# Kernel optimization log

Measured on AMD Instinct MI355X. Metric: run time of the kernel, lower is better.

The kernel has to match this reference:

```python
import jax, jax.numpy as jnp
import numpy as np

NL, NH, H, FF, V, P = 12, 12, 768, 3072, 30522, 512
B, L, S = 4, 512, 8
DH = H // NH


def _layer_norm(x, g, b, eps=1e-12):
    m = x.mean(-1, keepdims=True)
    v = jnp.mean((x - m) ** 2, axis=-1, keepdims=True)
    return (x - m) * jax.lax.rsqrt(v + eps) * g + b


def setup_inputs() -> dict:
    key = jax.random.key(0)
    ks = iter(jax.random.split(key, 40))
    pm = lambda shape: jax.random.normal(next(ks), shape, jnp.float32) * 0.02
    inp = {
        'word_emb': pm((V, H)), 'pos_emb': pm((P, H)), 'type_emb': pm((2, H)),
        'emb_ln_g': jnp.ones((H,), jnp.float32), 'emb_ln_b': jnp.zeros((H,), jnp.float32),
        'Wq': pm((NL, H, H)), 'bq': jnp.zeros((NL, H), jnp.float32),
        'Wk': pm((NL, H, H)), 'bk': jnp.zeros((NL, H), jnp.float32),
        'Wv': pm((NL, H, H)), 'bv': jnp.zeros((NL, H), jnp.float32),
        'Wo': pm((NL, H, H)), 'bo': jnp.zeros((NL, H), jnp.float32),
        'attn_ln_g': jnp.ones((NL, H), jnp.float32), 'attn_ln_b': jnp.zeros((NL, H), jnp.float32),
        'W1': pm((NL, H, FF)), 'b1': jnp.zeros((NL, FF), jnp.float32),
        'W2': pm((NL, FF, H)), 'b2': jnp.zeros((NL, H), jnp.float32),
        'ffn_ln_g': jnp.ones((NL, H), jnp.float32), 'ffn_ln_b': jnp.zeros((NL, H), jnp.float32),
        'fc_w': pm((H,)), 'fc_b': jnp.zeros((), jnp.float32),
    }
    inp['input_ids'] = jax.random.randint(next(ks), (B, L), 0, V)
    inp['token_type_ids'] = jnp.zeros((B, L), jnp.int32)
    # valid-length prefix attention_mask and sorted bos_locations (history = 64)
    vl = np.array([384 + 16 * (i % 8) for i in range(B)])
    hist = 64
    am = (np.arange(L)[None, :] < vl[:, None]).astype(np.int32)
    bos = np.stack([hist + (np.arange(S) * (v - hist)) // S for v in vl]).astype(np.int64)
    inp['attention_mask'] = jnp.asarray(am)
    inp['bos_locations'] = jnp.asarray(bos)
    return inp


def _forward(word_emb, pos_emb, type_emb, emb_ln_g, emb_ln_b,
             Wq, bq, Wk, bk, Wv, bv, Wo, bo, attn_ln_g, attn_ln_b,
             W1, b1, W2, b2, ffn_ln_g, ffn_ln_b, fc_w, fc_b,
             input_ids, token_type_ids, attention_mask, bos_locations):
    Bs, Ls = input_ids.shape
    t = jnp.arange(Ls)
    valid_len = attention_mask.sum(-1)                       # [B]
    hist = bos_locations[:, 0]                               # [B] history length
    # segment id per token: number of bos positions <= t, minus 1 (-1 in history)
    seg = (bos_locations[:, :, None] <= t[None, None, :]).sum(1) - 1   # [B,L]
    valid = t[None, :] < valid_len[:, None]                  # [B,L]
    # block-diagonal candidate attention mask (history rows/cols fully visible)
    p = t[None, :, None]
    q = t[None, None, :]
    hist_pq = (p < hist[:, None, None]) | (q < hist[:, None, None])
    same_seg = seg[:, :, None] == seg[:, None, :]
    mask = valid[:, :, None] & valid[:, None, :] & (hist_pq | same_seg)  # [B,L,L]
    bias = jnp.where(mask, 0.0, -10000.0).astype(jnp.float32)[:, None, :, :]  # [B,1,L,L]

    # BERT embeddings
    x = word_emb[input_ids] + pos_emb[t][None] + type_emb[token_type_ids]
    x = _layer_norm(x, emb_ln_g, emb_ln_b)
    scale = 1.0 / jnp.sqrt(jnp.asarray(DH, x.dtype))

    for l in range(NL):
        qh = (x @ Wq[l] + bq[l]).reshape(Bs, Ls, NH, DH)
        kh = (x @ Wk[l] + bk[l]).reshape(Bs, Ls, NH, DH)
        vh = (x @ Wv[l] + bv[l]).reshape(Bs, Ls, NH, DH)
        scores = jnp.einsum('bqhd,bkhd->bhqk', qh, kh) * scale + bias
        probs = jax.nn.softmax(scores, axis=-1)
        ctx = jnp.einsum('bhqk,bkhd->bqhd', probs, vh).reshape(Bs, Ls, H)
        x = _layer_norm(x + ctx @ Wo[l] + bo[l], attn_ln_g[l], attn_ln_b[l])
        h = jax.nn.gelu(x @ W1[l] + b1[l], approximate=False)
        x = _layer_norm(x + h @ W2[l] + b2[l], ffn_ln_g[l], ffn_ln_b[l])

    # variable-length segment mean pooling via membership matmul
    starts = bos_locations                                   # [B,S]
    ends = jnp.concatenate([bos_locations[:, 1:], valid_len[:, None]], axis=1)
    memb = ((t[None, None, :] >= starts[:, :, None]) &
            (t[None, None, :] < ends[:, :, None])).astype(x.dtype)        # [B,S,L]
    pooled = jnp.einsum('bsl,bld->bsd', memb, x) / memb.sum(-1, keepdims=True)
    logits = pooled @ fc_w + fc_b                            # [B,S]
    return jnp.squeeze(logits)


def reference(word_emb, pos_emb, type_emb, emb_ln_g, emb_ln_b,
              Wq, bq, Wk, bk, Wv, bv, Wo, bo, attn_ln_g, attn_ln_b,
              W1, b1, W2, b2, ffn_ln_g, ffn_ln_b, fc_w, fc_b,
              input_ids, token_type_ids, attention_mask, bos_locations):
    return _forward(word_emb, pos_emb, type_emb, emb_ln_g, emb_ln_b,
                    Wq, bq, Wk, bk, Wv, bv, Wo, bo, attn_ln_g, attn_ln_b,
                    W1, b1, W2, b2, ffn_ln_g, ffn_ln_b, fc_w, fc_b,
                    input_ids, token_type_ids, attention_mask, bos_locations)
```

## Files before the change

kernel.cpp:

```cpp
#include <hip/hip_runtime.h>
#include <math.h>

#define HH 768
#define FF 3072
#define NL 12
#define NH 12
#define DH 64
#define BB 4
#define LL 512
#define SS 8
#define MM (BB*LL)
#define WQSZ (HH*HH)
#define W1SZ (HH*FF)
#define LWB 7077888
#define OFF_WO 1769472
#define OFF_W1 2359296
#define OFF_W2 4718592

typedef short bf16x8 __attribute__((ext_vector_type(8)));
typedef float f32x4 __attribute__((ext_vector_type(4)));

__device__ inline ushort f2b(float f) {
  unsigned u = __float_as_uint(f);
  unsigned r = (u + 0x7FFFu + ((u >> 16) & 1u)) >> 16;
  return (ushort)r;
}
__device__ inline float b2f(ushort b) {
  return __uint_as_float(((unsigned)b) << 16);
}

__device__ inline void swz_xy(int& x, int& y) {
  int gx = gridDim.x, gy = gridDim.y;
  int flat = blockIdx.x + blockIdx.y * gx;
  int nwg = gx * gy;
  int q = nwg >> 3, r = nwg & 7;
  int xcd = flat & 7, off = flat >> 3;
  int wgid = (xcd < r ? xcd * (q + 1) : r * (q + 1) + (xcd - r) * q) + off;
  x = wgid / gy; y = wgid - x * gy;
}

__global__ void prep_kernel(const int* __restrict__ am, const int* __restrict__ bos,
                            int* __restrict__ seg, int* __restrict__ vl) {
  int b = blockIdx.x;
  int t = threadIdx.x;
  __shared__ int red[512];
  red[t] = am[b*LL + t];
  __syncthreads();
  for (int off = 256; off > 0; off >>= 1) {
    if (t < off) red[t] += red[t+off];
    __syncthreads();
  }
  if (t == 0) vl[b] = red[0];
  int cnt = 0;
  #pragma unroll
  for (int s = 0; s < SS; s++) cnt += (bos[b*SS + s] <= t) ? 1 : 0;
  seg[b*LL + t] = cnt - 1;
}

__global__ __launch_bounds__(256) void embed_ln_kernel(
    const float* __restrict__ word_emb, const float* __restrict__ pos_emb,
    const float* __restrict__ type_emb, const float* __restrict__ g,
    const float* __restrict__ bta, const int* __restrict__ ids,
    const int* __restrict__ tts, float* __restrict__ x, ushort* __restrict__ xb)
{
  int row = blockIdx.x;
  int l = row & (LL-1);
  int t = threadIdx.x;
  int id = ids[row];
  int ty = tts[row];
  float4 v = {0.f,0.f,0.f,0.f};
  float s = 0.f, sq = 0.f;
  int c = t << 2;
  if (t < 192) {
    float4 a = *(const float4*)&word_emb[(size_t)id*HH + c];
    float4 p = *(const float4*)&pos_emb[l*HH + c];
    float4 ttv = *(const float4*)&type_emb[ty*HH + c];
    v.x = a.x+p.x+ttv.x; v.y = a.y+p.y+ttv.y; v.z = a.z+p.z+ttv.z; v.w = a.w+p.w+ttv.w;
    s = v.x+v.y+v.z+v.w;
    sq = v.x*v.x+v.y*v.y+v.z*v.z+v.w*v.w;
  }
  __shared__ float rs[256], rq[256];
  rs[t] = s; rq[t] = sq;
  __syncthreads();
  for (int off = 128; off > 0; off >>= 1) {
    if (t < off) { rs[t] += rs[t+off]; rq[t] += rq[t+off]; }
    __syncthreads();
  }
  float mean = rs[0] / HH;
  float var  = rq[0] / HH - mean*mean;
  float inv  = rsqrtf(var + 1e-12f);
  if (t < 192) {
    float4 gv = *(const float4*)&g[c];
    float4 bv = *(const float4*)&bta[c];
    float4 o;
    o.x = (v.x-mean)*inv*gv.x + bv.x;
    o.y = (v.y-mean)*inv*gv.y + bv.y;
    o.z = (v.z-mean)*inv*gv.z + bv.z;
    o.w = (v.w-mean)*inv*gv.w + bv.w;
    *(float4*)&x[(size_t)row*HH + c] = o;
    ushort4 ob = { f2b(o.x), f2b(o.y), f2b(o.z), f2b(o.w) };
    *(ushort4*)&xb[(size_t)row*HH + c] = ob;
  }
}

template<int NP>
__global__ __launch_bounds__(256) void add_ln_kernel(
    const float* __restrict__ xin, const ushort* __restrict__ y,
    const float* __restrict__ g, const float* __restrict__ bta,
    float* __restrict__ xout, ushort* __restrict__ xb)
{
  int row = blockIdx.x;
  int t = threadIdx.x;
  float4 v = {0.f,0.f,0.f,0.f};
  float s = 0.f, sq = 0.f;
  int c = t << 2;
  size_t ix = (size_t)row*HH + c;
  if (t < 192) {
    v = *(const float4*)&xin[ix];
    #pragma unroll
    for (int p = 0; p < NP; p++) {
      ushort4 yb = *(const ushort4*)&y[(size_t)p*MM*HH + ix];
      v.x += b2f(yb.x); v.y += b2f(yb.y); v.z += b2f(yb.z); v.w += b2f(yb.w);
    }
    s = v.x+v.y+v.z+v.w;
    sq = v.x*v.x+v.y*v.y+v.z*v.z+v.w*v.w;
  }
  __shared__ float rs[256], rq[256];
  rs[t] = s; rq[t] = sq;
  __syncthreads();
  for (int off = 128; off > 0; off >>= 1) {
    if (t < off) { rs[t] += rs[t+off]; rq[t] += rq[t+off]; }
    __syncthreads();
  }
  float mean = rs[0] / HH;
  float var  = rq[0] / HH - mean*mean;
  float inv  = rsqrtf(var + 1e-12f);
  if (t < 192) {
    float4 gv = *(const float4*)&g[c];
    float4 bv = *(const float4*)&bta[c];
    float4 o;
    o.x = (v.x-mean)*inv*gv.x + bv.x;
    o.y = (v.y-mean)*inv*gv.y + bv.y;
    o.z = (v.z-mean)*inv*gv.z + bv.z;
    o.w = (v.w-mean)*inv*gv.w + bv.w;
    *(float4*)&xout[ix] = o;
    ushort4 ob = { f2b(o.x), f2b(o.y), f2b(o.z), f2b(o.w) };
    *(ushort4*)&xb[ix] = ob;
  }
}

__global__ __launch_bounds__(256) void convw_all_kernel(
    const float* __restrict__ Wq, const float* __restrict__ Wk,
    const float* __restrict__ Wv, const float* __restrict__ Wo,
    const float* __restrict__ W1, const float* __restrict__ W2,
    ushort* __restrict__ wbuf)
{
  int idx = blockIdx.x;
  int l = idx / 1728;
  int t0 = idx % 1728;
  size_t base = (size_t)l * LWB;
  const float* src; ushort* dst; int Nsrc, dstK, k0, n0src, n0dst;
  if (t0 < 432) {
    int nt = t0 / 12, kt = t0 % 12;
    int z = nt / 12, ntl = nt % 12;
    src = (z == 0 ? Wq : z == 1 ? Wk : Wv) + (size_t)l*WQSZ;
    dst = wbuf + base;
    Nsrc = HH; dstK = HH; k0 = kt*64; n0src = ntl*64; n0dst = nt*64;
  } else if (t0 < 576) {
    int t = t0 - 432; int nt = t / 12, kt = t % 12;
    src = Wo + (size_t)l*WQSZ;
    dst = wbuf + base + OFF_WO;
    Nsrc = HH; dstK = HH; k0 = kt*64; n0src = n0dst = nt*64;
  } else if (t0 < 1152) {
    int t = t0 - 576; int nt = t / 12, kt = t % 12;
    src = W1 + (size_t)l*W1SZ;
    dst = wbuf + base + OFF_W1;
    Nsrc = FF; dstK = HH; k0 = kt*64; n0src = n0dst = nt*64;
  } else {
    int t = t0 - 1152; int nt = t / 48, kt = t % 48;
    src = W2 + (size_t)l*W1SZ;
    dst = wbuf + base + OFF_W2;
    Nsrc = HH; dstK = FF; k0 = kt*64; n0src = n0dst = nt*64;
  }
  __shared__ ushort tt[64][66];
  int tid = threadIdx.x;
  int kr = tid >> 4;
  int nn0 = (tid & 15) << 2;
  #pragma unroll
  for (int i = 0; i < 4; i++) {
    int k = kr + i*16;
    float4 v = *(const float4*)&src[(size_t)(k0+k)*Nsrc + n0src + nn0];
    ushort2 lo = { f2b(v.x), f2b(v.y) };
    ushort2 hi = { f2b(v.z), f2b(v.w) };
    *(ushort2*)&tt[k][nn0]     = lo;
    *(ushort2*)&tt[k][nn0 + 2] = hi;
  }
  __syncthreads();
  ushort* dtile = dst + ((size_t)(n0dst >> 6)*(dstK >> 6) + (k0 >> 6)) * 4096;
  #pragma unroll
  for (int it = 0; it < 2; it++) {
    int n  = it*32 + (tid >> 3);
    int kc = (tid & 7) << 3;
    ushort tmp8[8];
    #pragma unroll
    for (int j = 0; j < 8; j++) tmp8[j] = tt[kc + j][n];
    *(uint4*)&dtile[n*64 + kc] = *(const uint4*)tmp8;
  }
}

template<int MODE>
__global__ __launch_bounds__(256) void gemm_bt(
    const ushort* __restrict__ A, const ushort* __restrict__ Bt,
    const float* __restrict__ ba, const float* __restrict__ bb,
    const float* __restrict__ bc, float* __restrict__ Cf,
    ushort* __restrict__ Cb, int M, int N, int K)
{
  __shared__ __align__(16) ushort As[2][128*64];
  __shared__ __align__(16) ushort Bs[2][64*64];
  const int tid = threadIdx.x;
  const int lane = tid & 63, wid = tid >> 6;
  const int wm = wid >> 1, wn = wid & 1;
  int bx, by; swz_xy(bx, by);
  const int m0 = by * 128, n0 = bx * 64;
  int kbeg = 0, kcnt = K;
  if (MODE == 2) { kcnt = K >> 1; kbeg = blockIdx.z * kcnt; }
  const int NT = kcnt >> 6;
  const ushort* Bpanel = Bt + (size_t)(n0 >> 6) * (K >> 6) * 4096;

  auto STAGE = [&](int buf, int k0) {
    #pragma unroll
    for (int j = 0; j < 4; j++) {
      int c = j*256 + tid;
      int r = c >> 3;
      int kk = ((c & 7) ^ (r & 7)) << 3;
      __builtin_amdgcn_global_load_lds(
        (const __attribute__((address_space(1))) void*)(A + (size_t)(m0+r)*K + k0 + kk),
        (__attribute__((address_space(3))) void*)(&As[buf][c*8]), 16, 0, 0);
    }
    const ushort* btile = Bpanel + (size_t)(k0 >> 6) * 4096;
    #pragma unroll
    for (int j = 0; j < 2; j++) {
      int c = j*256 + tid;
      int r = c >> 3;
      int kk = ((c & 7) ^ (r & 7)) << 3;
      __builtin_amdgcn_global_load_lds(
        (const __attribute__((address_space(1))) void*)(btile + r*64 + kk),
        (__attribute__((address_space(3))) void*)(&Bs[buf][c*8]), 16, 0, 0);
    }
  };

  f32x4 acc[4][2] = {};
  STAGE(0, kbeg);
  __syncthreads();
  int cur = 0;
  for (int t = 0; t < NT; ++t) {
    if (t + 1 < NT) STAGE(cur ^ 1, kbeg + (t+1)*64);
    bf16x8 af[4][2], bfv[2][2];
    #pragma unroll
    for (int mi = 0; mi < 4; mi++) {
      int row = wm*64 + mi*16 + (lane & 15);
      #pragma unroll
      for (int ks = 0; ks < 2; ks++) {
        int kb = (ks*64 + ((lane >> 4) << 4)) ^ ((row & 7) << 4);
        af[mi][ks] = *(const bf16x8*)((const char*)&As[cur][0] + row*128 + kb);
      }
    }
    #pragma unroll
    for (int ni = 0; ni < 2; ni++) {
      int row = wn*32 + ni*16 + (lane & 15);
      #pragma unroll
      for (int ks = 0; ks < 2; ks++) {
        int kb = (ks*64 + ((lane >> 4) << 4)) ^ ((row & 7) << 4);
        bfv[ni][ks] = *(const bf16x8*)((const char*)&Bs[cur][0] + row*128 + kb);
      }
    }
    #pragma unroll
    for (int ks = 0; ks < 2; ks++)
      #pragma unroll
      for (int mi = 0; mi < 4; mi++)
        #pragma unroll
        for (int ni = 0; ni < 2; ni++)
          acc[mi][ni] = __builtin_amdgcn_mfma_f32_16x16x32_bf16(af[mi][ks], bfv[ni][ks], acc[mi][ni], 0, 0, 0);
    __syncthreads();
    cur ^= 1;
  }

  #pragma unroll
  for (int mi = 0; mi < 4; mi++) {
    #pragma unroll
    for (int ni = 0; ni < 2; ni++) {
      int col = n0 + wn*32 + ni*16 + (lane & 15);
      if (MODE == 0) {
        int z = n0 / 768;
        int cc = col - z*768;
        float bvv = (z == 0 ? ba : z == 1 ? bb : bc)[cc];
        #pragma unroll
        for (int r = 0; r < 4; r++) {
          int row = m0 + wm*64 + mi*16 + (lane >> 4)*4 + r;
          Cb[(size_t)z*MM*HH + (size_t)row*HH + cc] = f2b(acc[mi][ni][r] + bvv);
        }
      } else if (MODE == 1) {
        float bvv = ba[col];
        #pragma unroll
        for (int r = 0; r < 4; r++) {
          int row = m0 + wm*64 + mi*16 + (lane >> 4)*4 + r;
          float v = acc[mi][ni][r] + bvv;
          v = 0.5f * v * (1.0f + erff(v * 0.70710678118654752f));
          Cb[(size_t)row*N + col] = f2b(v);
        }
      } else {
        float bvv = (blockIdx.z == 0) ? ba[col] : 0.f;
        #pragma unroll
        for (int r = 0; r < 4; r++) {
          int row = m0 + wm*64 + mi*16 + (lane >> 4)*4 + r;
          Cb[(size_t)blockIdx.z*M*N + (size_t)row*N + col] = f2b(acc[mi][ni][r] + bvv);
        }
      }
    }
  }
}

__global__ __launch_bounds__(256) void attn_mfma_kernel(
    const ushort* __restrict__ Q, const ushort* __restrict__ Kp, const ushort* __restrict__ Vp,
    ushort* __restrict__ ctx, const int* __restrict__ seg, const int* __restrict__ vl,
    const int* __restrict__ bos)
{
  const int q0 = blockIdx.x * 64;
  const int h  = blockIdx.y;
  const int b  = blockIdx.z;
  const int tid = threadIdx.x;
  const int lane = tid & 63;
  const int wid = tid >> 6;

  __shared__ __align__(16) char Ks[2][8192];
  __shared__ __align__(16) char Vt[2][8192];
  __shared__ __align__(16) char Ps[4][2048];
  __shared__ int segk[2][64];

  const int qrow_frag = q0 + wid*16 + (lane & 15);
  bf16x8 qf[2];
  #pragma unroll
  for (int c = 0; c < 2; c++)
    qf[c] = *(const bf16x8*)&Q[((size_t)(b*LL + qrow_frag))*HH + h*DH + 32*c + (lane >> 4)*8];

  const int vlb  = vl[b];
  const int hist = bos[b*SS];
  int segq[4]; bool qvalid[4], qhist[4];
  #pragma unroll
  for (int r = 0; r < 4; r++) {
    int qg = q0 + wid*16 + (lane >> 4)*4 + r;
    segq[r]   = seg[b*LL + qg];
    qvalid[r] = qg < vlb;
    qhist[r]  = qg < hist;
  }

  float mrow[4], lrow[4];
  #pragma unroll
  for (int r = 0; r < 4; r++) { mrow[r] = -1e30f; lrow[r] = 0.f; }
  f32x4 Oacc[4] = {};

  uint4 kreg0, kreg1, vreg0, vreg1;
  int sreg = 0;

  auto LOADT = [&](int k0) {
    int rk = tid >> 3;
    int c8 = (tid & 7) * 8;
    kreg0 = *(const uint4*)&Kp[((size_t)(b*LL + k0 + rk))*HH + h*DH + c8];
    kreg1 = *(const uint4*)&Kp[((size_t)(b*LL + k0 + rk + 32))*HH + h*DH + c8];
    vreg0 = *(const uint4*)&Vp[((size_t)(b*LL + k0 + lane))*HH + h*DH + wid*8];
    vreg1 = *(const uint4*)&Vp[((size_t)(b*LL + k0 + lane))*HH + h*DH + wid*8 + 32];
    if (tid < 64) sreg = seg[b*LL + k0 + tid];
  };
  auto STORET = [&](int buf) {
    int rk = tid >> 3;
    int c8 = (tid & 7) * 8;
    *(uint4*)(Ks[buf] + (rk*128 + ((c8*2) ^ ((rk & 7) << 4)))) = kreg0;
    int rk2 = rk + 32;
    *(uint4*)(Ks[buf] + (rk2*128 + ((c8*2) ^ ((rk2 & 7) << 4)))) = kreg1;
    const ushort* pv0 = (const ushort*)&vreg0;
    const ushort* pv1 = (const ushort*)&vreg1;
    #pragma unroll
    for (int j = 0; j < 8; j++) {
      int d  = wid*8 + j;
      *(ushort*)(Vt[buf] + (d*128 + ((lane*2) ^ ((d & 7) << 4)))) = pv0[j];
      int d2 = d + 32;
      *(ushort*)(Vt[buf] + (d2*128 + ((lane*2) ^ ((d2 & 7) << 4)))) = pv1[j];
    }
    if (tid < 64) segk[buf][tid] = sreg;
  };

  LOADT(0);
  STORET(0);
  __syncthreads();

  for (int kt = 0; kt < 8; kt++) {
    const int cur = kt & 1;
    const int k0 = kt * 64;
    if (kt < 7) LOADT(k0 + 64);
    __builtin_amdgcn_sched_barrier(0);

    f32x4 sacc[4] = {};
    #pragma unroll
    for (int t = 0; t < 4; t++) {
      int krow = (lane & 15) + 16*t;
      #pragma unroll
      for (int c = 0; c < 2; c++) {
        bf16x8 kf = *(const bf16x8*)(Ks[cur] + (krow*128 +
                      (((32*c + (lane >> 4)*8)*2) ^ ((krow & 7) << 4))));
        sacc[t] = __builtin_amdgcn_mfma_f32_16x16x32_bf16(qf[c], kf, sacc[t], 0, 0, 0);
      }
    }

    #pragma unroll
    for (int t = 0; t < 4; t++) {
      int kg = k0 + (lane & 15) + 16*t;
      bool kvalid = kg < vlb;
      bool khist  = kg < hist;
      int  sk     = segk[cur][(lane & 15) + 16*t];
      #pragma unroll
      for (int r = 0; r < 4; r++) {
        bool ok = qvalid[r] && kvalid && (khist || qhist[r] || (segq[r] == sk));
        sacc[t][r] = sacc[t][r]*0.125f + (ok ? 0.f : -10000.f);
      }
    }

    float scl[4];
    #pragma unroll
    for (int r = 0; r < 4; r++) {
      float rm = fmaxf(fmaxf(sacc[0][r], sacc[1][r]), fmaxf(sacc[2][r], sacc[3][r]));
      rm = fmaxf(rm, __shfl_xor(rm, 1));
      rm = fmaxf(rm, __shfl_xor(rm, 2));
      rm = fmaxf(rm, __shfl_xor(rm, 4));
      rm = fmaxf(rm, __shfl_xor(rm, 8));
      float mnew = (rm > mrow[r] + 8.f) ? rm : mrow[r];
      scl[r] = (mnew == mrow[r]) ? 1.f : __expf(mrow[r] - mnew);
      float rsum = 0.f;
      #pragma unroll
      for (int t = 0; t < 4; t++) {
        float p = __expf(sacc[t][r] - mnew);
        sacc[t][r] = p;
        rsum += p;
      }
      rsum += __shfl_xor(rsum, 1);
      rsum += __shfl_xor(rsum, 2);
      rsum += __shfl_xor(rsum, 4);
      rsum += __shfl_xor(rsum, 8);
      mrow[r] = mnew;
      lrow[r] = lrow[r]*scl[r] + rsum;
    }

    char* Pl = Ps[wid];
    #pragma unroll
    for (int t = 0; t < 4; t++) {
      #pragma unroll
      for (int r = 0; r < 4; r++) {
        int q = (lane >> 4)*4 + r;
        int k = (lane & 15) + 16*t;
        *(ushort*)(Pl + (q*128 + ((k*2) ^ ((q & 7) << 4)))) = f2b(sacc[t][r]);
      }
    }
    asm volatile("s_waitcnt lgkmcnt(0)" ::: "memory");
    bf16x8 pf[2];
    #pragma unroll
    for (int c = 0; c < 2; c++) {
      int q = lane & 15;
      int k = 32*c + (lane >> 4)*8;
      pf[c] = *(const bf16x8*)(Pl + (q*128 + ((k*2) ^ ((q & 7) << 4))));
    }

    bool needscale = (scl[0] != 1.f) | (scl[1] != 1.f) | (scl[2] != 1.f) | (scl[3] != 1.f);
    #pragma unroll
    for (int nt = 0; nt < 4; nt++) {
      if (needscale) {
        #pragma unroll
        for (int r = 0; r < 4; r++) Oacc[nt][r] *= scl[r];
      }
      int d = (lane & 15) + 16*nt;
      #pragma unroll
      for (int c = 0; c < 2; c++) {
        int k = 32*c + (lane >> 4)*8;
        bf16x8 vf = *(const bf16x8*)(Vt[cur] + (d*128 + ((k*2) ^ ((d & 7) << 4))));
        Oacc[nt] = __builtin_amdgcn_mfma_f32_16x16x32_bf16(pf[c], vf, Oacc[nt], 0, 0, 0);
      }
    }

    if (kt < 7) STORET(cur ^ 1);
    __syncthreads();
  }

  #pragma unroll
  for (int nt = 0; nt < 4; nt++) {
    #pragma unroll
    for (int r = 0; r < 4; r++) {
      int q = q0 + wid*16 + (lane >> 4)*4 + r;
      int d = h*DH + (lane & 15) + 16*nt;
      ctx[(size_t)(b*LL + q)*HH + d] = f2b(Oacc[nt][r] / lrow[r]);
    }
  }
}

__global__ __launch_bounds__(256) void rowdot_kernel(const float* __restrict__ x,
                                                     const float* __restrict__ w,
                                                     float* __restrict__ rd) {
  int row = blockIdx.x;
  int t = threadIdx.x;
  float s = 0.f;
  if (t < 192) {
    int c = t << 2;
    float4 xv = *(const float4*)&x[(size_t)row*HH + c];
    float4 wv = *(const float4*)&w[c];
    s = xv.x*wv.x + xv.y*wv.y + xv.z*wv.z + xv.w*wv.w;
  }
  __shared__ float red[256];
  red[t] = s;
  __syncthreads();
  for (int off = 128; off > 0; off >>= 1) {
    if (t < off) red[t] += red[t+off];
    __syncthreads();
  }
  if (t == 0) rd[row] = red[0];
}

__global__ void logits_kernel(const float* __restrict__ rd, const int* __restrict__ bos,
                              const int* __restrict__ vl, const float* __restrict__ fcb,
                              float* __restrict__ out) {
  int i = threadIdx.x;
  if (i >= BB*SS) return;
  int b = i / SS, s = i % SS;
  int start = bos[b*SS + s];
  int end   = (s == SS-1) ? vl[b] : bos[b*SS + s + 1];
  float sum = 0.f;
  for (int t = start; t < end; t++) sum += rd[b*LL + t];
  out[i] = sum / (float)(end - start) + fcb[0];
}

extern "C" void kernel_launch(void* const* d_in, const int* in_sizes, int n_in,
                              void* d_out, int out_size, void* d_ws, size_t ws_size,
                              hipStream_t stream) {
  const float* word_emb  = (const float*)d_in[0];
  const float* pos_emb   = (const float*)d_in[1];
  const float* type_emb  = (const float*)d_in[2];
  const float* emb_ln_g  = (const float*)d_in[3];
  const float* emb_ln_b  = (const float*)d_in[4];
  const float* Wq        = (const float*)d_in[5];
  const float* bq        = (const float*)d_in[6];
  const float* Wk        = (const float*)d_in[7];
  const float* bk        = (const float*)d_in[8];
  const float* Wv        = (const float*)d_in[9];
  const float* bv        = (const float*)d_in[10];
  const float* Wo        = (const float*)d_in[11];
  const float* bo        = (const float*)d_in[12];
  const float* attn_ln_g = (const float*)d_in[13];
  const float* attn_ln_b = (const float*)d_in[14];
  const float* W1        = (const float*)d_in[15];
  const float* b1        = (const float*)d_in[16];
  const float* W2        = (const float*)d_in[17];
  const float* b2        = (const float*)d_in[18];
  const float* ffn_ln_g  = (const float*)d_in[19];
  const float* ffn_ln_b  = (const float*)d_in[20];
  const float* fc_w      = (const float*)d_in[21];
  const float* fc_b      = (const float*)d_in[22];
  const int* input_ids   = (const int*)d_in[23];
  const int* token_type  = (const int*)d_in[24];
  const int* am          = (const int*)d_in[25];
  const int* bos         = (const int*)d_in[26];
  float* out = (float*)d_out;

  char* w = (char*)d_ws;
  float*  x       = (float*)w;  w += (size_t)MM*HH*4;
  ushort* tmpb    = (ushort*)w; w += (size_t)2*MM*HH*2;
  ushort* qkv_bf  = (ushort*)w; w += (size_t)3*MM*HH*2;
  ushort* x_bf    = (ushort*)w; w += (size_t)MM*HH*2;
  ushort* ctx_bf  = (ushort*)w; w += (size_t)MM*HH*2;
  ushort* hbuf_bf = (ushort*)w; w += (size_t)MM*FF*2;
  ushort* wbuf    = (ushort*)w; w += (size_t)NL*LWB*2;
  float*  rd      = (float*)w;  w += (size_t)MM*4;
  int*    seg     = (int*)w;    w += (size_t)MM*4;
  int*    vl      = (int*)w;    w += 64;

  prep_kernel<<<BB, 512, 0, stream>>>(am, bos, seg, vl);
  convw_all_kernel<<<NL*1728, 256, 0, stream>>>(Wq, Wk, Wv, Wo, W1, W2, wbuf);
  embed_ln_kernel<<<MM, 256, 0, stream>>>(word_emb, pos_emb, type_emb,
                                          emb_ln_g, emb_ln_b, input_ids, token_type, x, x_bf);

  dim3 gqkv(2304/64, MM/128);
  dim3 g_ff1(FF/64, MM/128);
  dim3 g_sk(HH/64, MM/128, 2);
  dim3 gattn(LL/64, NH, BB);

  for (int l = 0; l < NL; l++) {
    const ushort* Wqkv_t = wbuf + (size_t)l*LWB;
    const ushort* Wo_t   = wbuf + (size_t)l*LWB + OFF_WO;
    const ushort* W1_t   = wbuf + (size_t)l*LWB + OFF_W1;
    const ushort* W2_t   = wbuf + (size_t)l*LWB + OFF_W2;

    gemm_bt<0><<<gqkv, 256, 0, stream>>>(x_bf, Wqkv_t,
        bq + (size_t)l*HH, bk + (size_t)l*HH, bv + (size_t)l*HH,
        nullptr, qkv_bf, MM, 2304, HH);

    attn_mfma_kernel<<<gattn, 256, 0, stream>>>(qkv_bf, qkv_bf + (size_t)MM*HH,
                                                qkv_bf + (size_t)2*MM*HH, ctx_bf, seg, vl, bos);

    gemm_bt<2><<<g_sk, 256, 0, stream>>>(ctx_bf, Wo_t,
        bo + (size_t)l*HH, nullptr, nullptr, nullptr, tmpb, MM, HH, HH);

    add_ln_kernel<2><<<MM, 256, 0, stream>>>(x, tmpb, attn_ln_g + (size_t)l*HH,
                                             attn_ln_b + (size_t)l*HH, x, x_bf);

    gemm_bt<1><<<g_ff1, 256, 0, stream>>>(x_bf, W1_t,
        b1 + (size_t)l*FF, nullptr, nullptr, nullptr, hbuf_bf, MM, FF, HH);

    gemm_bt<2><<<g_sk, 256, 0, stream>>>(hbuf_bf, W2_t,
        b2 + (size_t)l*HH, nullptr, nullptr, nullptr, tmpb, MM, HH, FF);

    add_ln_kernel<2><<<MM, 256, 0, stream>>>(x, tmpb, ffn_ln_g + (size_t)l*HH,
                                             ffn_ln_b + (size_t)l*HH, x, x_bf);
  }

  rowdot_kernel<<<MM, 256, 0, stream>>>(x, fc_w, rd);
  logits_kernel<<<1, 64, 0, stream>>>(rd, bos, vl, fc_b, out);
}
```

Measured before the change: 1.439 ms.

## Split-K into four fp32 partials for Wo/W2 GEMMs and per-layer weight conversion

```diff
diff --git a/kernel.cpp b/kernel.cpp
--- a/kernel.cpp
+++ b/kernel.cpp
@@ -24,9 +24,6 @@
   unsigned u = __float_as_uint(f);
   unsigned r = (u + 0x7FFFu + ((u >> 16) & 1u)) >> 16;
   return (ushort)r;
-}
-__device__ inline float b2f(ushort b) {
-  return __uint_as_float(((unsigned)b) << 16);
 }
 
 __device__ inline void swz_xy(int& x, int& y) {
@@ -105,7 +102,7 @@
 
 template<int NP>
 __global__ __launch_bounds__(256) void add_ln_kernel(
-    const float* __restrict__ xin, const ushort* __restrict__ y,
+    const float* __restrict__ xin, const float* __restrict__ y,
     const float* __restrict__ g, const float* __restrict__ bta,
     float* __restrict__ xout, ushort* __restrict__ xb)
 {
@@ -119,8 +116,8 @@
     v = *(const float4*)&xin[ix];
     #pragma unroll
     for (int p = 0; p < NP; p++) {
-      ushort4 yb = *(const ushort4*)&y[(size_t)p*MM*HH + ix];
-      v.x += b2f(yb.x); v.y += b2f(yb.y); v.z += b2f(yb.z); v.w += b2f(yb.w);
+      float4 yv = *(const float4*)&y[(size_t)p*MM*HH + ix];
+      v.x += yv.x; v.y += yv.y; v.z += yv.z; v.w += yv.w;
     }
     s = v.x+v.y+v.z+v.w;
     sq = v.x*v.x+v.y*v.y+v.z*v.z+v.w*v.w;
@@ -149,37 +146,31 @@
   }
 }
 
-__global__ __launch_bounds__(256) void convw_all_kernel(
+__global__ __launch_bounds__(256) void convw_layer_kernel(
     const float* __restrict__ Wq, const float* __restrict__ Wk,
     const float* __restrict__ Wv, const float* __restrict__ Wo,
     const float* __restrict__ W1, const float* __restrict__ W2,
-    ushort* __restrict__ wbuf)
+    ushort* __restrict__ wl)
 {
-  int idx = blockIdx.x;
-  int l = idx / 1728;
-  int t0 = idx % 1728;
-  size_t base = (size_t)l * LWB;
+  int t0 = blockIdx.x;
   const float* src; ushort* dst; int Nsrc, dstK, k0, n0src, n0dst;
   if (t0 < 432) {
     int nt = t0 / 12, kt = t0 % 12;
     int z = nt / 12, ntl = nt % 12;
-    src = (z == 0 ? Wq : z == 1 ? Wk : Wv) + (size_t)l*WQSZ;
-    dst = wbuf + base;
+    src = (z == 0 ? Wq : z == 1 ? Wk : Wv);
+    dst = wl;
     Nsrc = HH; dstK = HH; k0 = kt*64; n0src = ntl*64; n0dst = nt*64;
   } else if (t0 < 576) {
     int t = t0 - 432; int nt = t / 12, kt = t % 12;
-    src = Wo + (size_t)l*WQSZ;
-    dst = wbuf + base + OFF_WO;
+    src = Wo; dst = wl + OFF_WO;
     Nsrc = HH; dstK = HH; k0 = kt*64; n0src = n0dst = nt*64;
   } else if (t0 < 1152) {
     int t = t0 - 576; int nt = t / 12, kt = t % 12;
-    src = W1 + (size_t)l*W1SZ;
-    dst = wbuf + base + OFF_W1;
+    src = W1; dst = wl + OFF_W1;
     Nsrc = FF; dstK = HH; k0 = kt*64; n0src = n0dst = nt*64;
   } else {
     int t = t0 - 1152; int nt = t / 48, kt = t % 48;
-    src = W2 + (size_t)l*W1SZ;
-    dst = wbuf + base + OFF_W2;
+    src = W2; dst = wl + OFF_W2;
     Nsrc = HH; dstK = FF; k0 = kt*64; n0src = n0dst = nt*64;
   }
   __shared__ ushort tt[64][66];
@@ -223,7 +214,7 @@
   int bx, by; swz_xy(bx, by);
   const int m0 = by * 128, n0 = bx * 64;
   int kbeg = 0, kcnt = K;
-  if (MODE == 2) { kcnt = K >> 1; kbeg = blockIdx.z * kcnt; }
+  if (MODE == 2) { kcnt = K >> 2; kbeg = blockIdx.z * kcnt; }
   const int NT = kcnt >> 6;
   const ushort* Bpanel = Bt + (size_t)(n0 >> 6) * (K >> 6) * 4096;
 
@@ -313,7 +304,7 @@
         #pragma unroll
         for (int r = 0; r < 4; r++) {
           int row = m0 + wm*64 + mi*16 + (lane >> 4)*4 + r;
-          Cb[(size_t)blockIdx.z*M*N + (size_t)row*N + col] = f2b(acc[mi][ni][r] + bvv);
+          Cf[(size_t)blockIdx.z*M*N + (size_t)row*N + col] = acc[mi][ni][r] + bvv;
         }
       }
     }
@@ -568,7 +559,7 @@
 
   char* w = (char*)d_ws;
   float*  x       = (float*)w;  w += (size_t)MM*HH*4;
-  ushort* tmpb    = (ushort*)w; w += (size_t)2*MM*HH*2;
+  float*  tmp     = (float*)w;  w += (size_t)4*MM*HH*4;
   ushort* qkv_bf  = (ushort*)w; w += (size_t)3*MM*HH*2;
   ushort* x_bf    = (ushort*)w; w += (size_t)MM*HH*2;
   ushort* ctx_bf  = (ushort*)w; w += (size_t)MM*HH*2;
@@ -579,13 +570,17 @@
   int*    vl      = (int*)w;    w += 64;
 
   prep_kernel<<<BB, 512, 0, stream>>>(am, bos, seg, vl);
-  convw_all_kernel<<<NL*1728, 256, 0, stream>>>(Wq, Wk, Wv, Wo, W1, W2, wbuf);
+  for (int l = 0; l < NL; l++)
+    convw_layer_kernel<<<1728, 256, 0, stream>>>(
+        Wq + (size_t)l*WQSZ, Wk + (size_t)l*WQSZ, Wv + (size_t)l*WQSZ,
+        Wo + (size_t)l*WQSZ, W1 + (size_t)l*W1SZ, W2 + (size_t)l*W1SZ,
+        wbuf + (size_t)l*LWB);
   embed_ln_kernel<<<MM, 256, 0, stream>>>(word_emb, pos_emb, type_emb,
                                           emb_ln_g, emb_ln_b, input_ids, token_type, x, x_bf);
 
   dim3 gqkv(2304/64, MM/128);
   dim3 g_ff1(FF/64, MM/128);
-  dim3 g_sk(HH/64, MM/128, 2);
+  dim3 g_sk(HH/64, MM/128, 4);
   dim3 gattn(LL/64, NH, BB);
 
   for (int l = 0; l < NL; l++) {
@@ -602,18 +597,18 @@
                                                 qkv_bf + (size_t)2*MM*HH, ctx_bf, seg, vl, bos);
 
     gemm_bt<2><<<g_sk, 256, 0, stream>>>(ctx_bf, Wo_t,
-        bo + (size_t)l*HH, nullptr, nullptr, nullptr, tmpb, MM, HH, HH);
-
-    add_ln_kernel<2><<<MM, 256, 0, stream>>>(x, tmpb, attn_ln_g + (size_t)l*HH,
+        bo + (size_t)l*HH, nullptr, nullptr, tmp, nullptr, MM, HH, HH);
+
+    add_ln_kernel<4><<<MM, 256, 0, stream>>>(x, tmp, attn_ln_g + (size_t)l*HH,
                                              attn_ln_b + (size_t)l*HH, x, x_bf);
 
     gemm_bt<1><<<g_ff1, 256, 0, stream>>>(x_bf, W1_t,
         b1 + (size_t)l*FF, nullptr, nullptr, nullptr, hbuf_bf, MM, FF, HH);
 
     gemm_bt<2><<<g_sk, 256, 0, stream>>>(hbuf_bf, W2_t,
-        b2 + (size_t)l*HH, nullptr, nullptr, nullptr, tmpb, MM, HH, FF);
-
-    add_ln_kernel<2><<<MM, 256, 0, stream>>>(x, tmpb, ffn_ln_g + (size_t)l*HH,
+        b2 + (size_t)l*HH, nullptr, nullptr, tmp, nullptr, MM, HH, FF);
+
+    add_ln_kernel<4><<<MM, 256, 0, stream>>>(x, tmp, ffn_ln_g + (size_t)l*HH,
                                              ffn_ln_b + (size_t)l*HH, x, x_bf);
   }
 
```

New measurement: 1.442 ms. Within noise of the previous version (+0.2%).

## Deepen GEMM prefetch pipeline, use 4-way split-K with fp32 partials

Applied to the files above, without the earlier changes.

```diff
diff --git a/kernel.cpp b/kernel.cpp
--- a/kernel.cpp
+++ b/kernel.cpp
@@ -24,9 +24,6 @@
   unsigned u = __float_as_uint(f);
   unsigned r = (u + 0x7FFFu + ((u >> 16) & 1u)) >> 16;
   return (ushort)r;
-}
-__device__ inline float b2f(ushort b) {
-  return __uint_as_float(((unsigned)b) << 16);
 }
 
 __device__ inline void swz_xy(int& x, int& y) {
@@ -105,7 +102,7 @@
 
 template<int NP>
 __global__ __launch_bounds__(256) void add_ln_kernel(
-    const float* __restrict__ xin, const ushort* __restrict__ y,
+    const float* __restrict__ xin, const float* __restrict__ y,
     const float* __restrict__ g, const float* __restrict__ bta,
     float* __restrict__ xout, ushort* __restrict__ xb)
 {
@@ -119,8 +116,8 @@
     v = *(const float4*)&xin[ix];
     #pragma unroll
     for (int p = 0; p < NP; p++) {
-      ushort4 yb = *(const ushort4*)&y[(size_t)p*MM*HH + ix];
-      v.x += b2f(yb.x); v.y += b2f(yb.y); v.z += b2f(yb.z); v.w += b2f(yb.w);
+      float4 yv = *(const float4*)&y[(size_t)p*MM*HH + ix];
+      v.x += yv.x; v.y += yv.y; v.z += yv.z; v.w += yv.w;
     }
     s = v.x+v.y+v.z+v.w;
     sq = v.x*v.x+v.y*v.y+v.z*v.z+v.w*v.w;
@@ -223,7 +220,7 @@
   int bx, by; swz_xy(bx, by);
   const int m0 = by * 128, n0 = bx * 64;
   int kbeg = 0, kcnt = K;
-  if (MODE == 2) { kcnt = K >> 1; kbeg = blockIdx.z * kcnt; }
+  if (MODE == 2) { kcnt = K >> 2; kbeg = blockIdx.z * kcnt; }
   const int NT = kcnt >> 6;
   const ushort* Bpanel = Bt + (size_t)(n0 >> 6) * (K >> 6) * 4096;
 
@@ -251,10 +248,15 @@
 
   f32x4 acc[4][2] = {};
   STAGE(0, kbeg);
-  __syncthreads();
-  int cur = 0;
+  if (NT > 1) STAGE(1, kbeg + 64);
   for (int t = 0; t < NT; ++t) {
-    if (t + 1 < NT) STAGE(cur ^ 1, kbeg + (t+1)*64);
+    const int cur = t & 1;
+    if (t + 1 < NT) asm volatile("s_waitcnt vmcnt(6)" ::: "memory");
+    else            asm volatile("s_waitcnt vmcnt(0)" ::: "memory");
+    __builtin_amdgcn_sched_barrier(0);
+    __builtin_amdgcn_s_barrier();
+    __builtin_amdgcn_sched_barrier(0);
+
     bf16x8 af[4][2], bfv[2][2];
     #pragma unroll
     for (int mi = 0; mi < 4; mi++) {
@@ -281,8 +283,12 @@
         #pragma unroll
         for (int ni = 0; ni < 2; ni++)
           acc[mi][ni] = __builtin_amdgcn_mfma_f32_16x16x32_bf16(af[mi][ks], bfv[ni][ks], acc[mi][ni], 0, 0, 0);
-    __syncthreads();
-    cur ^= 1;
+
+    asm volatile("s_waitcnt lgkmcnt(0)" ::: "memory");
+    __builtin_amdgcn_sched_barrier(0);
+    __builtin_amdgcn_s_barrier();
+    __builtin_amdgcn_sched_barrier(0);
+    if (t + 2 < NT) STAGE(cur, kbeg + (t + 2) * 64);
   }
 
   #pragma unroll
@@ -313,7 +319,7 @@
         #pragma unroll
         for (int r = 0; r < 4; r++) {
           int row = m0 + wm*64 + mi*16 + (lane >> 4)*4 + r;
-          Cb[(size_t)blockIdx.z*M*N + (size_t)row*N + col] = f2b(acc[mi][ni][r] + bvv);
+          Cf[(size_t)blockIdx.z*M*N + (size_t)row*N + col] = acc[mi][ni][r] + bvv;
         }
       }
     }
@@ -568,7 +574,7 @@
 
   char* w = (char*)d_ws;
   float*  x       = (float*)w;  w += (size_t)MM*HH*4;
-  ushort* tmpb    = (ushort*)w; w += (size_t)2*MM*HH*2;
+  float*  tmp     = (float*)w;  w += (size_t)4*MM*HH*4;
   ushort* qkv_bf  = (ushort*)w; w += (size_t)3*MM*HH*2;
   ushort* x_bf    = (ushort*)w; w += (size_t)MM*HH*2;
   ushort* ctx_bf  = (ushort*)w; w += (size_t)MM*HH*2;
@@ -585,7 +591,7 @@
 
   dim3 gqkv(2304/64, MM/128);
   dim3 g_ff1(FF/64, MM/128);
-  dim3 g_sk(HH/64, MM/128, 2);
+  dim3 g_sk(HH/64, MM/128, 4);
   dim3 gattn(LL/64, NH, BB);
 
   for (int l = 0; l < NL; l++) {
@@ -602,18 +608,18 @@
                                                 qkv_bf + (size_t)2*MM*HH, ctx_bf, seg, vl, bos);
 
     gemm_bt<2><<<g_sk, 256, 0, stream>>>(ctx_bf, Wo_t,
-        bo + (size_t)l*HH, nullptr, nullptr, nullptr, tmpb, MM, HH, HH);
-
-    add_ln_kernel<2><<<MM, 256, 0, stream>>>(x, tmpb, attn_ln_g + (size_t)l*HH,
+        bo + (size_t)l*HH, nullptr, nullptr, tmp, nullptr, MM, HH, HH);
+
+    add_ln_kernel<4><<<MM, 256, 0, stream>>>(x, tmp, attn_ln_g + (size_t)l*HH,
                                              attn_ln_b + (size_t)l*HH, x, x_bf);
 
     gemm_bt<1><<<g_ff1, 256, 0, stream>>>(x_bf, W1_t,
         b1 + (size_t)l*FF, nullptr, nullptr, nullptr, hbuf_bf, MM, FF, HH);
 
     gemm_bt<2><<<g_sk, 256, 0, stream>>>(hbuf_bf, W2_t,
-        b2 + (size_t)l*HH, nullptr, nullptr, nullptr, tmpb, MM, HH, FF);
-
-    add_ln_kernel<2><<<MM, 256, 0, stream>>>(x, tmpb, ffn_ln_g + (size_t)l*HH,
+        b2 + (size_t)l*HH, nullptr, nullptr, tmp, nullptr, MM, HH, FF);
+
+    add_ln_kernel<4><<<MM, 256, 0, stream>>>(x, tmp, ffn_ln_g + (size_t)l*HH,
                                              ffn_ln_b + (size_t)l*HH, x, x_bf);
   }
 
```

Measured after the change: 1.420 ms. No clear change (-1.3%).
